# Kernel tuning notes

Measured on AMD Instinct MI355X. Metric: run time of the kernel, lower is better.

Reference implementation:

```python
import jax, jax.numpy as jnp
import numpy as np

B, T, D, H = 2, 2048, 1024, 16
HS = D // H  # head_size = 64
EPS = 1e-5


def layer_norm(x, g, b):
    mu = jnp.mean(x, axis=-1, keepdims=True)
    var = jnp.var(x, axis=-1, keepdims=True)
    return (x - mu) * jax.lax.rsqrt(var + EPS) * g + b


def setup_inputs() -> dict:
    key = jax.random.key(0)
    ks = jax.random.split(key, 12)
    s_attn = 1.0 / np.sqrt(D)
    s_ff1 = 1.0 / np.sqrt(D)
    s_ff2 = 1.0 / np.sqrt(4 * D)
    return {
        "x": jax.random.normal(ks[0], (B, T, D), jnp.float32),
        "Wq": jax.random.normal(ks[1], (H, D, HS), jnp.float32) * s_attn,
        "Wk": jax.random.normal(ks[2], (H, D, HS), jnp.float32) * s_attn,
        "Wv": jax.random.normal(ks[3], (H, D, HS), jnp.float32) * s_attn,
        "Wo": jax.random.normal(ks[4], (H * HS, D), jnp.float32) * (1.0 / np.sqrt(H * HS)),
        "bo": jnp.zeros((D,), jnp.float32),
        "W1": jax.random.normal(ks[5], (D, 4 * D), jnp.float32) * s_ff1,
        "b1": jnp.zeros((4 * D,), jnp.float32),
        "W2": jax.random.normal(ks[6], (4 * D, D), jnp.float32) * s_ff2,
        "b2": jnp.zeros((D,), jnp.float32),
        "ln1_g": jnp.ones((D,), jnp.float32),
        "ln1_b": jnp.zeros((D,), jnp.float32),
        "ln2_g": jnp.ones((D,), jnp.float32),
        "ln2_b": jnp.zeros((D,), jnp.float32),
    }


def reference(x, Wq, Wk, Wv, Wo, bo, W1, b1, W2, b2, ln1_g, ln1_b, ln2_g, ln2_b):
    # --- self-attention on ln1(x) ---
    h = layer_norm(x, ln1_g, ln1_b)
    Q = jnp.einsum('bsd,hdk->bhsk', h, Wq)
    K = jnp.einsum('bsd,hdk->bhsk', h, Wk)
    V = jnp.einsum('bsd,hdk->bhsk', h, Wv)
    scores = jnp.einsum('bhqk,bhsk->bhqs', Q, K) * (HS ** -0.5)
    attn = jax.nn.softmax(scores, axis=-1)  # [B,H,T,T] non-causal, as in source
    out = jnp.einsum('bhqs,bhsk->bhqk', attn, V)
    out = out.transpose(0, 2, 1, 3).reshape(B, T, H * HS)  # concat heads
    sa = out @ Wo + bo
    x = x + sa
    # --- feed-forward on ln2(x) ---
    h2 = layer_norm(x, ln2_g, ln2_b)
    ff = jax.nn.relu(h2 @ W1 + b1) @ W2 + b2
    return x + ff
```

## Files before the change

kernel.cpp:

```cpp
#include <hip/hip_runtime.h>
#include <cstdint>
#include <cmath>

typedef __bf16 bf16;
typedef __bf16 bf16x8 __attribute__((ext_vector_type(8)));
typedef __bf16 bf16x4 __attribute__((ext_vector_type(4)));
typedef float  f32x4  __attribute__((ext_vector_type(4)));

#define B_   2
#define T_   2048
#define D_   1024
#define H_   16
#define HS_  64
#define NTOK (B_ * T_)

typedef __attribute__((address_space(1))) uint8_t* gp1_t;
typedef __attribute__((address_space(3))) uint8_t* lp3_t;
__device__ __forceinline__ void gl_lds16(const void* g, void* l) {
    __builtin_amdgcn_global_load_lds((gp1_t)(uintptr_t)g,
                                     (lp3_t)(uint32_t)(uintptr_t)l,
                                     16, 0, 0);
}

__device__ __forceinline__ f32x4 mfma16(bf16x8 a, bf16x8 b, f32x4 c) {
    return __builtin_amdgcn_mfma_f32_16x16x32_bf16(a, b, c, 0, 0, 0);
}

__global__ void tcast(const float* __restrict__ in, bf16* __restrict__ out,
                      int R, int C) {
    __shared__ float t[32][33];
    const int c0 = blockIdx.x * 32, r0 = blockIdx.y * 32;
    for (int i = 0; i < 4; i++) {
        int r = threadIdx.y + i * 8;
        t[r][threadIdx.x] = in[(size_t)(r0 + r) * C + c0 + threadIdx.x];
    }
    __syncthreads();
    for (int i = 0; i < 4; i++) {
        int rr = threadIdx.y + i * 8;
        out[(size_t)(c0 + rr) * R + r0 + threadIdx.x] = (bf16)t[threadIdx.x][rr];
    }
}

__global__ void qkv_pack(const float* __restrict__ Wq, const float* __restrict__ Wk,
                         const float* __restrict__ Wv, bf16* __restrict__ out) {
    const int z = blockIdx.z;
    const int qkv = z >> 4;
    const float* in = (qkv == 0 ? Wq : qkv == 1 ? Wk : Wv) + (size_t)(z & 15) * D_ * HS_;
    bf16* o = out + (size_t)z * HS_ * D_;
    __shared__ float t[32][33];
    const int c0 = blockIdx.x * 32, r0 = blockIdx.y * 32;
    for (int i = 0; i < 4; i++) {
        int r = threadIdx.y + i * 8;
        t[r][threadIdx.x] = in[(size_t)(r0 + r) * HS_ + c0 + threadIdx.x];
    }
    __syncthreads();
    for (int i = 0; i < 4; i++) {
        int rr = threadIdx.y + i * 8;
        o[(size_t)(c0 + rr) * D_ + r0 + threadIdx.x] = (bf16)t[threadIdx.x][rr];
    }
}

__global__ void vt_pack(const bf16* __restrict__ QKV, bf16* __restrict__ Vt) {
    const int z = blockIdx.z;
    const int b = z >> 4, h = z & 15;
    const bf16* in = QKV + (size_t)b * T_ * 3072 + 2048 + h * 64;
    bf16* o = Vt + (size_t)z * HS_ * T_;
    __shared__ bf16 t[32][33];
    const int c0 = blockIdx.x * 32, r0 = blockIdx.y * 32;
    for (int i = 0; i < 4; i++) {
        int r = threadIdx.y + i * 8;
        t[r][threadIdx.x] = in[(size_t)(r0 + r) * 3072 + c0 + threadIdx.x];
    }
    __syncthreads();
    for (int i = 0; i < 4; i++) {
        int rr = threadIdx.y + i * 8;
        o[(size_t)(c0 + rr) * T_ + r0 + threadIdx.x] = t[threadIdx.x][rr];
    }
}

__global__ __launch_bounds__(256) void ln_kernel(const float* __restrict__ x,
                                                 const float* __restrict__ g,
                                                 const float* __restrict__ b,
                                                 bf16* __restrict__ out) {
    const int row = blockIdx.x;
    const int tid = threadIdx.x;
    const float4 v = ((const float4*)(x + (size_t)row * 1024))[tid];
    float s  = v.x + v.y + v.z + v.w;
    float s2 = v.x * v.x + v.y * v.y + v.z * v.z + v.w * v.w;
    for (int m = 1; m < 64; m <<= 1) {
        s  += __shfl_xor(s, m);
        s2 += __shfl_xor(s2, m);
    }
    __shared__ float rs[4], rq[4];
    const int lane = tid & 63, wv = tid >> 6;
    if (lane == 0) { rs[wv] = s; rq[wv] = s2; }
    __syncthreads();
    s  = rs[0] + rs[1] + rs[2] + rs[3];
    s2 = rq[0] + rq[1] + rq[2] + rq[3];
    const float mu   = s * (1.f / 1024.f);
    const float var  = s2 * (1.f / 1024.f) - mu * mu;
    const float rstd = rsqrtf(var + 1e-5f);
    const float4 gg = ((const float4*)g)[tid];
    const float4 bb = ((const float4*)b)[tid];
    bf16x4 o;
    o[0] = (bf16)((v.x - mu) * rstd * gg.x + bb.x);
    o[1] = (bf16)((v.y - mu) * rstd * gg.y + bb.y);
    o[2] = (bf16)((v.z - mu) * rstd * gg.z + bb.z);
    o[3] = (bf16)((v.w - mu) * rstd * gg.w + bb.w);
    *(bf16x4*)(out + (size_t)row * 1024 + tid * 4) = o;
}

__global__ __launch_bounds__(256) void combine2(const float* __restrict__ p0,
                                                const float* __restrict__ p1,
                                                const float* __restrict__ resid,
                                                const float* __restrict__ bias,
                                                float* __restrict__ out) {
    const int i4 = blockIdx.x * 256 + threadIdx.x;
    const float4 a = ((const float4*)p0)[i4];
    const float4 b = ((const float4*)p1)[i4];
    const float4 r = ((const float4*)resid)[i4];
    const float4 bb = ((const float4*)bias)[i4 & 255];
    float4 o;
    o.x = a.x + b.x + r.x + bb.x;
    o.y = a.y + b.y + r.y + bb.y;
    o.z = a.z + b.z + r.z + bb.z;
    o.w = a.w + b.w + r.w + bb.w;
    ((float4*)out)[i4] = o;
}

template <int BIAS, int RELU, int RES, int OUTBF16>
__global__ __launch_bounds__(256, 2) void gemm_bt(
    const bf16* __restrict__ A, const bf16* __restrict__ Bt,
    const float* __restrict__ bias, const float* __restrict__ resid,
    void* __restrict__ Cout, int M, int N, int K) {
    __shared__ __align__(16) bf16 As[128 * 32];
    __shared__ __align__(16) bf16 Bs[128 * 32];
    const int tid  = threadIdx.x;
    const int lane = tid & 63, w = tid >> 6;
    const int quad = lane >> 4, l15 = lane & 15;
    const int m0 = blockIdx.y * 128, n0 = blockIdx.x * 128;
    const int wm = (w & 1) * 64, wn = (w >> 1) * 64;

    f32x4 acc[4][4];
    for (int i = 0; i < 4; i++)
        for (int j = 0; j < 4; j++) acc[i][j] = f32x4{0.f, 0.f, 0.f, 0.f};

    const int arow = lane >> 2;
    const int acol = (lane & 3) * 8;
    const int c0 = w * 2, c1 = w * 2 + 1;

    for (int kt = 0; kt < K; kt += 32) {
        gl_lds16(A  + (size_t)(m0 + c0 * 16 + arow) * K + kt + acol, &As[c0 * 512]);
        gl_lds16(A  + (size_t)(m0 + c1 * 16 + arow) * K + kt + acol, &As[c1 * 512]);
        gl_lds16(Bt + (size_t)(n0 + c0 * 16 + arow) * K + kt + acol, &Bs[c0 * 512]);
        gl_lds16(Bt + (size_t)(n0 + c1 * 16 + arow) * K + kt + acol, &Bs[c1 * 512]);
        __syncthreads();
        bf16x8 af[4], bfr[4];
        for (int mi = 0; mi < 4; mi++)
            af[mi] = *(const bf16x8*)&As[(wm + mi * 16 + l15) * 32 + quad * 8];
        for (int ni = 0; ni < 4; ni++)
            bfr[ni] = *(const bf16x8*)&Bs[(wn + ni * 16 + l15) * 32 + quad * 8];
        for (int mi = 0; mi < 4; mi++)
            for (int ni = 0; ni < 4; ni++)
                acc[mi][ni] = mfma16(af[mi], bfr[ni], acc[mi][ni]);
        __syncthreads();
    }

    for (int mi = 0; mi < 4; mi++) {
        for (int ni = 0; ni < 4; ni++) {
            const int colb = n0 + wn + ni * 16 + l15;
            const float bv = BIAS ? bias[colb] : 0.f;
            for (int r = 0; r < 4; r++) {
                const int row = m0 + wm + mi * 16 + quad * 4 + r;
                float v = acc[mi][ni][r] + bv;
                if (RELU) v = fmaxf(v, 0.f);
                if (RES)  v += resid[(size_t)row * N + colb];
                if (OUTBF16) ((bf16*)Cout)[(size_t)row * N + colb] = (bf16)v;
                else         ((float*)Cout)[(size_t)row * N + colb] = v;
            }
        }
    }
}

__global__ __launch_bounds__(256, 2) void gemm_bt_partial(
    const bf16* __restrict__ A, const bf16* __restrict__ Bt,
    float* __restrict__ Cpart, int M, int N, int K) {
    __shared__ __align__(16) bf16 As[128 * 32];
    __shared__ __align__(16) bf16 Bs[128 * 32];
    const int tid  = threadIdx.x;
    const int lane = tid & 63, w = tid >> 6;
    const int quad = lane >> 4, l15 = lane & 15;
    const int m0 = blockIdx.y * 128, n0 = blockIdx.x * 128;
    const int wm = (w & 1) * 64, wn = (w >> 1) * 64;
    const int kpb = K / gridDim.z;
    const int k0 = blockIdx.z * kpb, k1 = k0 + kpb;
    float* Cz = Cpart + (size_t)blockIdx.z * M * N;

    f32x4 acc[4][4];
    for (int i = 0; i < 4; i++)
        for (int j = 0; j < 4; j++) acc[i][j] = f32x4{0.f, 0.f, 0.f, 0.f};

    const int arow = lane >> 2;
    const int acol = (lane & 3) * 8;
    const int c0 = w * 2, c1 = w * 2 + 1;

    for (int kt = k0; kt < k1; kt += 32) {
        gl_lds16(A  + (size_t)(m0 + c0 * 16 + arow) * K + kt + acol, &As[c0 * 512]);
        gl_lds16(A  + (size_t)(m0 + c1 * 16 + arow) * K + kt + acol, &As[c1 * 512]);
        gl_lds16(Bt + (size_t)(n0 + c0 * 16 + arow) * K + kt + acol, &Bs[c0 * 512]);
        gl_lds16(Bt + (size_t)(n0 + c1 * 16 + arow) * K + kt + acol, &Bs[c1 * 512]);
        __syncthreads();
        bf16x8 af[4], bfr[4];
        for (int mi = 0; mi < 4; mi++)
            af[mi] = *(const bf16x8*)&As[(wm + mi * 16 + l15) * 32 + quad * 8];
        for (int ni = 0; ni < 4; ni++)
            bfr[ni] = *(const bf16x8*)&Bs[(wn + ni * 16 + l15) * 32 + quad * 8];
        for (int mi = 0; mi < 4; mi++)
            for (int ni = 0; ni < 4; ni++)
                acc[mi][ni] = mfma16(af[mi], bfr[ni], acc[mi][ni]);
        __syncthreads();
    }

    for (int mi = 0; mi < 4; mi++) {
        for (int ni = 0; ni < 4; ni++) {
            const int colb = n0 + wn + ni * 16 + l15;
            for (int r = 0; r < 4; r++) {
                const int row = m0 + wm + mi * 16 + quad * 4 + r;
                Cz[(size_t)row * N + colb] = acc[mi][ni][r];
            }
        }
    }
}

#define LSTR 68
#define NJ   (T_ / 64)
__global__ __launch_bounds__(512, 2) void flash_attn(const bf16* __restrict__ QKV,
                                                     const bf16* __restrict__ Vt,
                                                     bf16* __restrict__ attn_out) {
    const int bh = blockIdx.y, b = bh >> 4, h = bh & 15;
    const int q0 = blockIdx.x * 256;
    const int tid = threadIdx.x, lane = tid & 63, w = tid >> 6;
    const int quad = lane >> 4, l15 = lane & 15;
    __shared__ __align__(16) bf16 Ks[2][64 * LSTR];
    __shared__ __align__(16) bf16 Vs[2][64 * LSTR];
    __shared__ __align__(16) bf16 Ps[256 * LSTR];
    const bf16* Qb = QKV + (size_t)b * T_ * 3072 + h * 64;
    const bf16* Kb = QKV + (size_t)b * T_ * 3072 + 1024 + h * 64;
    const bf16* Vb = Vt  + (size_t)bh * HS_ * T_;

    const float sc = 0.125f * 1.44269504088896f;
    const int sr = tid >> 3, scc = (tid & 7) * 8;

    bf16x8 QA[2][2];
    for (int qnt = 0; qnt < 2; qnt++) {
        const size_t row = (size_t)(q0 + w * 32 + qnt * 16 + l15) * 3072;
        for (int kk = 0; kk < 2; kk++) {
            bf16x8 q = *(const bf16x8*)&Qb[row + kk * 32 + quad * 8];
            for (int i = 0; i < 8; i++) q[i] = (bf16)((float)q[i] * sc);
            QA[qnt][kk] = q;
        }
    }

    bf16x8 ones8;
    for (int i = 0; i < 8; i++) ones8[i] = (bf16)1.0f;

    f32x4 O[2][4], lacc[2];
    for (int mi = 0; mi < 2; mi++) {
        lacc[mi] = f32x4{0.f, 0.f, 0.f, 0.f};
        for (int n = 0; n < 4; n++) O[mi][n] = f32x4{0.f, 0.f, 0.f, 0.f};
    }

    *(bf16x8*)&Ks[0][sr * LSTR + scc] = *(const bf16x8*)&Kb[(size_t)sr * 3072 + scc];
    *(bf16x8*)&Vs[0][sr * LSTR + scc] = *(const bf16x8*)&Vb[(size_t)sr * T_ + scc];
    __syncthreads();

    bf16x8 kreg, vreg;
    for (int j = 0; j < NJ; j++) {
        const int buf = j & 1;
        if (j + 1 < NJ) {
            const int s1 = (j + 1) * 64;
            kreg = *(const bf16x8*)&Kb[(size_t)(s1 + sr) * 3072 + scc];
            vreg = *(const bf16x8*)&Vb[(size_t)sr * T_ + s1 + scc];
        }
        bf16x8 KB[4][2];
        for (int smt = 0; smt < 4; smt++)
            for (int kk = 0; kk < 2; kk++)
                KB[smt][kk] = *(const bf16x8*)&Ks[buf][(smt * 16 + l15) * LSTR + kk * 32 + quad * 8];
        for (int qnt = 0; qnt < 2; qnt++) {
            f32x4 ST[4];
            for (int smt = 0; smt < 4; smt++) ST[smt] = f32x4{0.f, 0.f, 0.f, 0.f};
            for (int kk = 0; kk < 2; kk++)
                for (int smt = 0; smt < 4; smt++)
                    ST[smt] = mfma16(KB[smt][kk], QA[qnt][kk], ST[smt]);
            const int prow = (w * 32 + qnt * 16 + l15) * LSTR + quad * 4;
            for (int smt = 0; smt < 4; smt++) {
                bf16x4 p4;
                p4[0] = (bf16)__builtin_amdgcn_exp2f(ST[smt][0]);
                p4[1] = (bf16)__builtin_amdgcn_exp2f(ST[smt][1]);
                p4[2] = (bf16)__builtin_amdgcn_exp2f(ST[smt][2]);
                p4[3] = (bf16)__builtin_amdgcn_exp2f(ST[smt][3]);
                *(bf16x4*)&Ps[prow + smt * 16] = p4;
            }
        }
        bf16x8 VB[4][2];
        for (int n = 0; n < 4; n++)
            for (int kk = 0; kk < 2; kk++)
                VB[n][kk] = *(const bf16x8*)&Vs[buf][(n * 16 + l15) * LSTR + kk * 32 + quad * 8];
        for (int mi = 0; mi < 2; mi++) {
            const int pr = (w * 32 + mi * 16 + l15) * LSTR + quad * 8;
            bf16x8 PA0 = *(const bf16x8*)&Ps[pr];
            bf16x8 PA1 = *(const bf16x8*)&Ps[pr + 32];
            for (int n = 0; n < 4; n++) {
                O[mi][n] = mfma16(PA0, VB[n][0], O[mi][n]);
                O[mi][n] = mfma16(PA1, VB[n][1], O[mi][n]);
            }
            lacc[mi] = mfma16(PA0, ones8, lacc[mi]);
            lacc[mi] = mfma16(PA1, ones8, lacc[mi]);
        }
        if (j + 1 < NJ) {
            *(bf16x8*)&Ks[buf ^ 1][sr * LSTR + scc] = kreg;
            *(bf16x8*)&Vs[buf ^ 1][sr * LSTR + scc] = vreg;
        }
        __syncthreads();
    }

    for (int mi = 0; mi < 2; mi++) {
        for (int r = 0; r < 4; r++) {
            const float inv = 1.f / lacc[mi][r];
            const size_t tok = (size_t)b * T_ + q0 + w * 32 + mi * 16 + quad * 4 + r;
            for (int n = 0; n < 4; n++)
                attn_out[tok * 1024 + h * 64 + n * 16 + l15] = (bf16)(O[mi][n][r] * inv);
        }
    }
}

extern "C" void kernel_launch(void* const* d_in, const int* in_sizes, int n_in,
                              void* d_out, int out_size, void* d_ws, size_t ws_size,
                              hipStream_t stream) {
    const float* x   = (const float*)d_in[0];
    const float* Wq  = (const float*)d_in[1];
    const float* Wk  = (const float*)d_in[2];
    const float* Wv  = (const float*)d_in[3];
    const float* Wo  = (const float*)d_in[4];
    const float* bo  = (const float*)d_in[5];
    const float* W1  = (const float*)d_in[6];
    const float* b1  = (const float*)d_in[7];
    const float* W2  = (const float*)d_in[8];
    const float* b2  = (const float*)d_in[9];
    const float* g1  = (const float*)d_in[10];
    const float* be1 = (const float*)d_in[11];
    const float* g2  = (const float*)d_in[12];
    const float* be2 = (const float*)d_in[13];

    char* ws = (char*)d_ws;
    const size_t MB = 1ull << 20;
    bf16*  WqkvT = (bf16*)(ws);
    bf16*  WoT   = (bf16*)(ws + 6  * MB);
    bf16*  W1T   = (bf16*)(ws + 8  * MB);
    bf16*  W2T   = (bf16*)(ws + 16 * MB);
    bf16*  hbuf  = (bf16*)(ws + 24 * MB);
    bf16*  QKV   = (bf16*)(ws + 32 * MB);
    bf16*  Vt    = (bf16*)(ws + 56 * MB);
    bf16*  attn  = (bf16*)(ws + 64 * MB);
    float* x2    = (float*)(ws + 72 * MB);
    bf16*  ff1   = (bf16*)(ws + 32 * MB);
    float* part  = (float*)(ws + 88 * MB);
    float* out   = (float*)d_out;

    dim3 tb(32, 8);
    qkv_pack<<<dim3(2, 32, 48), tb, 0, stream>>>(Wq, Wk, Wv, WqkvT);
    tcast<<<dim3(32, 32),  tb, 0, stream>>>(Wo, WoT, 1024, 1024);
    tcast<<<dim3(128, 32), tb, 0, stream>>>(W1, W1T, 1024, 4096);
    tcast<<<dim3(32, 128), tb, 0, stream>>>(W2, W2T, 4096, 1024);
    ln_kernel<<<NTOK, 256, 0, stream>>>(x, g1, be1, hbuf);
    gemm_bt<0, 0, 0, 1><<<dim3(24, 32), 256, 0, stream>>>(hbuf, WqkvT, nullptr, nullptr, QKV, NTOK, 3072, 1024);
    vt_pack<<<dim3(2, 64, 32), tb, 0, stream>>>(QKV, Vt);
    flash_attn<<<dim3(T_ / 256, B_ * H_), 512, 0, stream>>>(QKV, Vt, attn);
    gemm_bt<1, 0, 1, 0><<<dim3(8, 32), 256, 0, stream>>>(attn, WoT, bo, x, x2, NTOK, 1024, 1024);
    ln_kernel<<<NTOK, 256, 0, stream>>>(x2, g2, be2, hbuf);
    gemm_bt<1, 1, 0, 1><<<dim3(32, 32), 256, 0, stream>>>(hbuf, W1T, b1, nullptr, ff1, NTOK, 4096, 1024);
    gemm_bt_partial<<<dim3(8, 32, 2), 256, 0, stream>>>(ff1, W2T, part, NTOK, 1024, 4096);
    combine2<<<NTOK, 256, 0, stream>>>(part, part + (size_t)NTOK * 1024, x2, b2, out);
}
```

Before: 353.7 us.

## Fuse V transpose into QKV GEMM epilogue, double K-step in GEMMs, shrink attention blocks

The QKV GEMM epilogue now writes the V columns directly in transposed layout to Vt, which removes the separate vt_pack kernel and its extra pass over memory. Both GEMM kernels now load 64 K-elements per barrier pair instead of 32, halving the number of syncs at the cost of doubling LDS use. Flash attention moves to 256-thread blocks covering 128 queries each, with each thread staging 16 elements of K/V. This gives twice as many blocks, aiming at better occupancy and load balance.

```diff
diff --git a/kernel.cpp b/kernel.cpp
--- a/kernel.cpp
+++ b/kernel.cpp
@@ -57,24 +57,6 @@
     for (int i = 0; i < 4; i++) {
         int rr = threadIdx.y + i * 8;
         o[(size_t)(c0 + rr) * D_ + r0 + threadIdx.x] = (bf16)t[threadIdx.x][rr];
-    }
-}
-
-__global__ void vt_pack(const bf16* __restrict__ QKV, bf16* __restrict__ Vt) {
-    const int z = blockIdx.z;
-    const int b = z >> 4, h = z & 15;
-    const bf16* in = QKV + (size_t)b * T_ * 3072 + 2048 + h * 64;
-    bf16* o = Vt + (size_t)z * HS_ * T_;
-    __shared__ bf16 t[32][33];
-    const int c0 = blockIdx.x * 32, r0 = blockIdx.y * 32;
-    for (int i = 0; i < 4; i++) {
-        int r = threadIdx.y + i * 8;
-        t[r][threadIdx.x] = in[(size_t)(r0 + r) * 3072 + c0 + threadIdx.x];
-    }
-    __syncthreads();
-    for (int i = 0; i < 4; i++) {
-        int rr = threadIdx.y + i * 8;
-        o[(size_t)(c0 + rr) * T_ + r0 + threadIdx.x] = t[threadIdx.x][rr];
     }
 }
 
@@ -128,13 +110,13 @@
     ((float4*)out)[i4] = o;
 }
 
-template <int BIAS, int RELU, int RES, int OUTBF16>
+template <int BIAS, int RELU, int RES, int OUTBF16, int VTP = 0>
 __global__ __launch_bounds__(256, 2) void gemm_bt(
     const bf16* __restrict__ A, const bf16* __restrict__ Bt,
     const float* __restrict__ bias, const float* __restrict__ resid,
-    void* __restrict__ Cout, int M, int N, int K) {
-    __shared__ __align__(16) bf16 As[128 * 32];
-    __shared__ __align__(16) bf16 Bs[128 * 32];
+    void* __restrict__ Cout, bf16* __restrict__ Vt, int M, int N, int K) {
+    __shared__ __align__(16) bf16 As[2][128 * 32];
+    __shared__ __align__(16) bf16 Bs[2][128 * 32];
     const int tid  = threadIdx.x;
     const int lane = tid & 63, w = tid >> 6;
     const int quad = lane >> 4, l15 = lane & 15;
@@ -149,26 +131,44 @@
     const int acol = (lane & 3) * 8;
     const int c0 = w * 2, c1 = w * 2 + 1;
 
-    for (int kt = 0; kt < K; kt += 32) {
-        gl_lds16(A  + (size_t)(m0 + c0 * 16 + arow) * K + kt + acol, &As[c0 * 512]);
-        gl_lds16(A  + (size_t)(m0 + c1 * 16 + arow) * K + kt + acol, &As[c1 * 512]);
-        gl_lds16(Bt + (size_t)(n0 + c0 * 16 + arow) * K + kt + acol, &Bs[c0 * 512]);
-        gl_lds16(Bt + (size_t)(n0 + c1 * 16 + arow) * K + kt + acol, &Bs[c1 * 512]);
-        __syncthreads();
-        bf16x8 af[4], bfr[4];
-        for (int mi = 0; mi < 4; mi++)
-            af[mi] = *(const bf16x8*)&As[(wm + mi * 16 + l15) * 32 + quad * 8];
-        for (int ni = 0; ni < 4; ni++)
-            bfr[ni] = *(const bf16x8*)&Bs[(wn + ni * 16 + l15) * 32 + quad * 8];
-        for (int mi = 0; mi < 4; mi++)
+    for (int kt = 0; kt < K; kt += 64) {
+        gl_lds16(A  + (size_t)(m0 + c0 * 16 + arow) * K + kt + acol,      &As[0][c0 * 512]);
+        gl_lds16(A  + (size_t)(m0 + c1 * 16 + arow) * K + kt + acol,      &As[0][c1 * 512]);
+        gl_lds16(A  + (size_t)(m0 + c0 * 16 + arow) * K + kt + 32 + acol, &As[1][c0 * 512]);
+        gl_lds16(A  + (size_t)(m0 + c1 * 16 + arow) * K + kt + 32 + acol, &As[1][c1 * 512]);
+        gl_lds16(Bt + (size_t)(n0 + c0 * 16 + arow) * K + kt + acol,      &Bs[0][c0 * 512]);
+        gl_lds16(Bt + (size_t)(n0 + c1 * 16 + arow) * K + kt + acol,      &Bs[0][c1 * 512]);
+        gl_lds16(Bt + (size_t)(n0 + c0 * 16 + arow) * K + kt + 32 + acol, &Bs[1][c0 * 512]);
+        gl_lds16(Bt + (size_t)(n0 + c1 * 16 + arow) * K + kt + 32 + acol, &Bs[1][c1 * 512]);
+        __syncthreads();
+        for (int kh = 0; kh < 2; kh++) {
+            bf16x8 af[4], bfr[4];
+            for (int mi = 0; mi < 4; mi++)
+                af[mi] = *(const bf16x8*)&As[kh][(wm + mi * 16 + l15) * 32 + quad * 8];
             for (int ni = 0; ni < 4; ni++)
-                acc[mi][ni] = mfma16(af[mi], bfr[ni], acc[mi][ni]);
+                bfr[ni] = *(const bf16x8*)&Bs[kh][(wn + ni * 16 + l15) * 32 + quad * 8];
+            for (int mi = 0; mi < 4; mi++)
+                for (int ni = 0; ni < 4; ni++)
+                    acc[mi][ni] = mfma16(af[mi], bfr[ni], acc[mi][ni]);
+        }
         __syncthreads();
     }
 
     for (int mi = 0; mi < 4; mi++) {
         for (int ni = 0; ni < 4; ni++) {
             const int colb = n0 + wn + ni * 16 + l15;
+            if (VTP && colb >= 2048) {
+                const int h = (colb - 2048) >> 6, hs = (colb - 2048) & 63;
+                const int row0 = m0 + wm + mi * 16 + quad * 4;
+                const int b = row0 >> 11;
+                bf16x4 p4;
+                p4[0] = (bf16)acc[mi][ni][0];
+                p4[1] = (bf16)acc[mi][ni][1];
+                p4[2] = (bf16)acc[mi][ni][2];
+                p4[3] = (bf16)acc[mi][ni][3];
+                *(bf16x4*)&Vt[((size_t)(b * 16 + h) * 64 + hs) * T_ + (row0 & 2047)] = p4;
+                continue;
+            }
             const float bv = BIAS ? bias[colb] : 0.f;
             for (int r = 0; r < 4; r++) {
                 const int row = m0 + wm + mi * 16 + quad * 4 + r;
@@ -185,8 +185,8 @@
 __global__ __launch_bounds__(256, 2) void gemm_bt_partial(
     const bf16* __restrict__ A, const bf16* __restrict__ Bt,
     float* __restrict__ Cpart, int M, int N, int K) {
-    __shared__ __align__(16) bf16 As[128 * 32];
-    __shared__ __align__(16) bf16 Bs[128 * 32];
+    __shared__ __align__(16) bf16 As[2][128 * 32];
+    __shared__ __align__(16) bf16 Bs[2][128 * 32];
     const int tid  = threadIdx.x;
     const int lane = tid & 63, w = tid >> 6;
     const int quad = lane >> 4, l15 = lane & 15;
@@ -204,20 +204,26 @@
     const int acol = (lane & 3) * 8;
     const int c0 = w * 2, c1 = w * 2 + 1;
 
-    for (int kt = k0; kt < k1; kt += 32) {
-        gl_lds16(A  + (size_t)(m0 + c0 * 16 + arow) * K + kt + acol, &As[c0 * 512]);
-        gl_lds16(A  + (size_t)(m0 + c1 * 16 + arow) * K + kt + acol, &As[c1 * 512]);
-        gl_lds16(Bt + (size_t)(n0 + c0 * 16 + arow) * K + kt + acol, &Bs[c0 * 512]);
-        gl_lds16(Bt + (size_t)(n0 + c1 * 16 + arow) * K + kt + acol, &Bs[c1 * 512]);
-        __syncthreads();
-        bf16x8 af[4], bfr[4];
-        for (int mi = 0; mi < 4; mi++)
-            af[mi] = *(const bf16x8*)&As[(wm + mi * 16 + l15) * 32 + quad * 8];
-        for (int ni = 0; ni < 4; ni++)
-            bfr[ni] = *(const bf16x8*)&Bs[(wn + ni * 16 + l15) * 32 + quad * 8];
-        for (int mi = 0; mi < 4; mi++)
+    for (int kt = k0; kt < k1; kt += 64) {
+        gl_lds16(A  + (size_t)(m0 + c0 * 16 + arow) * K + kt + acol,      &As[0][c0 * 512]);
+        gl_lds16(A  + (size_t)(m0 + c1 * 16 + arow) * K + kt + acol,      &As[0][c1 * 512]);
+        gl_lds16(A  + (size_t)(m0 + c0 * 16 + arow) * K + kt + 32 + acol, &As[1][c0 * 512]);
+        gl_lds16(A  + (size_t)(m0 + c1 * 16 + arow) * K + kt + 32 + acol, &As[1][c1 * 512]);
+        gl_lds16(Bt + (size_t)(n0 + c0 * 16 + arow) * K + kt + acol,      &Bs[0][c0 * 512]);
+        gl_lds16(Bt + (size_t)(n0 + c1 * 16 + arow) * K + kt + acol,      &Bs[0][c1 * 512]);
+        gl_lds16(Bt + (size_t)(n0 + c0 * 16 + arow) * K + kt + 32 + acol, &Bs[1][c0 * 512]);
+        gl_lds16(Bt + (size_t)(n0 + c1 * 16 + arow) * K + kt + 32 + acol, &Bs[1][c1 * 512]);
+        __syncthreads();
+        for (int kh = 0; kh < 2; kh++) {
+            bf16x8 af[4], bfr[4];
+            for (int mi = 0; mi < 4; mi++)
+                af[mi] = *(const bf16x8*)&As[kh][(wm + mi * 16 + l15) * 32 + quad * 8];
             for (int ni = 0; ni < 4; ni++)
-                acc[mi][ni] = mfma16(af[mi], bfr[ni], acc[mi][ni]);
+                bfr[ni] = *(const bf16x8*)&Bs[kh][(wn + ni * 16 + l15) * 32 + quad * 8];
+            for (int mi = 0; mi < 4; mi++)
+                for (int ni = 0; ni < 4; ni++)
+                    acc[mi][ni] = mfma16(af[mi], bfr[ni], acc[mi][ni]);
+        }
         __syncthreads();
     }
 
@@ -234,22 +240,22 @@
 
 #define LSTR 68
 #define NJ   (T_ / 64)
-__global__ __launch_bounds__(512, 2) void flash_attn(const bf16* __restrict__ QKV,
+__global__ __launch_bounds__(256, 2) void flash_attn(const bf16* __restrict__ QKV,
                                                      const bf16* __restrict__ Vt,
                                                      bf16* __restrict__ attn_out) {
     const int bh = blockIdx.y, b = bh >> 4, h = bh & 15;
-    const int q0 = blockIdx.x * 256;
+    const int q0 = blockIdx.x * 128;
     const int tid = threadIdx.x, lane = tid & 63, w = tid >> 6;
     const int quad = lane >> 4, l15 = lane & 15;
     __shared__ __align__(16) bf16 Ks[2][64 * LSTR];
     __shared__ __align__(16) bf16 Vs[2][64 * LSTR];
-    __shared__ __align__(16) bf16 Ps[256 * LSTR];
+    __shared__ __align__(16) bf16 Ps[128 * LSTR];
     const bf16* Qb = QKV + (size_t)b * T_ * 3072 + h * 64;
     const bf16* Kb = QKV + (size_t)b * T_ * 3072 + 1024 + h * 64;
     const bf16* Vb = Vt  + (size_t)bh * HS_ * T_;
 
     const float sc = 0.125f * 1.44269504088896f;
-    const int sr = tid >> 3, scc = (tid & 7) * 8;
+    const int sr = tid >> 2, scc = (tid & 3) * 16;
 
     bf16x8 QA[2][2];
     for (int qnt = 0; qnt < 2; qnt++) {
@@ -270,17 +276,21 @@
         for (int n = 0; n < 4; n++) O[mi][n] = f32x4{0.f, 0.f, 0.f, 0.f};
     }
 
-    *(bf16x8*)&Ks[0][sr * LSTR + scc] = *(const bf16x8*)&Kb[(size_t)sr * 3072 + scc];
-    *(bf16x8*)&Vs[0][sr * LSTR + scc] = *(const bf16x8*)&Vb[(size_t)sr * T_ + scc];
+    *(bf16x8*)&Ks[0][sr * LSTR + scc]     = *(const bf16x8*)&Kb[(size_t)sr * 3072 + scc];
+    *(bf16x8*)&Ks[0][sr * LSTR + scc + 8] = *(const bf16x8*)&Kb[(size_t)sr * 3072 + scc + 8];
+    *(bf16x8*)&Vs[0][sr * LSTR + scc]     = *(const bf16x8*)&Vb[(size_t)sr * T_ + scc];
+    *(bf16x8*)&Vs[0][sr * LSTR + scc + 8] = *(const bf16x8*)&Vb[(size_t)sr * T_ + scc + 8];
     __syncthreads();
 
-    bf16x8 kreg, vreg;
+    bf16x8 k0, k1, v0, v1;
     for (int j = 0; j < NJ; j++) {
         const int buf = j & 1;
         if (j + 1 < NJ) {
             const int s1 = (j + 1) * 64;
-            kreg = *(const bf16x8*)&Kb[(size_t)(s1 + sr) * 3072 + scc];
-            vreg = *(const bf16x8*)&Vb[(size_t)sr * T_ + s1 + scc];
+            k0 = *(const bf16x8*)&Kb[(size_t)(s1 + sr) * 3072 + scc];
+            k1 = *(const bf16x8*)&Kb[(size_t)(s1 + sr) * 3072 + scc + 8];
+            v0 = *(const bf16x8*)&Vb[(size_t)sr * T_ + s1 + scc];
+            v1 = *(const bf16x8*)&Vb[(size_t)sr * T_ + s1 + scc + 8];
         }
         bf16x8 KB[4][2];
         for (int smt = 0; smt < 4; smt++)
@@ -318,8 +328,10 @@
             lacc[mi] = mfma16(PA1, ones8, lacc[mi]);
         }
         if (j + 1 < NJ) {
-            *(bf16x8*)&Ks[buf ^ 1][sr * LSTR + scc] = kreg;
-            *(bf16x8*)&Vs[buf ^ 1][sr * LSTR + scc] = vreg;
+            *(bf16x8*)&Ks[buf ^ 1][sr * LSTR + scc]     = k0;
+            *(bf16x8*)&Ks[buf ^ 1][sr * LSTR + scc + 8] = k1;
+            *(bf16x8*)&Vs[buf ^ 1][sr * LSTR + scc]     = v0;
+            *(bf16x8*)&Vs[buf ^ 1][sr * LSTR + scc + 8] = v1;
         }
         __syncthreads();
     }
@@ -373,12 +385,11 @@
     tcast<<<dim3(128, 32), tb, 0, stream>>>(W1, W1T, 1024, 4096);
     tcast<<<dim3(32, 128), tb, 0, stream>>>(W2, W2T, 4096, 1024);
     ln_kernel<<<NTOK, 256, 0, stream>>>(x, g1, be1, hbuf);
-    gemm_bt<0, 0, 0, 1><<<dim3(24, 32), 256, 0, stream>>>(hbuf, WqkvT, nullptr, nullptr, QKV, NTOK, 3072, 1024);
-    vt_pack<<<dim3(2, 64, 32), tb, 0, stream>>>(QKV, Vt);
-    flash_attn<<<dim3(T_ / 256, B_ * H_), 512, 0, stream>>>(QKV, Vt, attn);
-    gemm_bt<1, 0, 1, 0><<<dim3(8, 32), 256, 0, stream>>>(attn, WoT, bo, x, x2, NTOK, 1024, 1024);
+    gemm_bt<0, 0, 0, 1, 1><<<dim3(24, 32), 256, 0, stream>>>(hbuf, WqkvT, nullptr, nullptr, QKV, Vt, NTOK, 3072, 1024);
+    flash_attn<<<dim3(T_ / 128, B_ * H_), 256, 0, stream>>>(QKV, Vt, attn);
+    gemm_bt<1, 0, 1, 0><<<dim3(8, 32), 256, 0, stream>>>(attn, WoT, bo, x, x2, nullptr, NTOK, 1024, 1024);
     ln_kernel<<<NTOK, 256, 0, stream>>>(x2, g2, be2, hbuf);
-    gemm_bt<1, 1, 0, 1><<<dim3(32, 32), 256, 0, stream>>>(hbuf, W1T, b1, nullptr, ff1, NTOK, 4096, 1024);
+    gemm_bt<1, 1, 0, 1><<<dim3(32, 32), 256, 0, stream>>>(hbuf, W1T, b1, nullptr, ff1, nullptr, NTOK, 4096, 1024);
     gemm_bt_partial<<<dim3(8, 32, 2), 256, 0, stream>>>(ff1, W2T, part, NTOK, 1024, 4096);
     combine2<<<NTOK, 256, 0, stream>>>(part, part + (size_t)NTOK * 1024, x2, b2, out);
 }
```

New measurement: 340.3 us. -3.8%, faster.
